# Kernel optimization log

Hardware: AMD Instinct MI355X
Metric: run time of the kernel (lower is better)

The kernel has to match this reference:

```python
import jax, jax.numpy as jnp
import numpy as np

N_PATCHES = 262144
N_BAGS = 32
INPUT_DIM = 1024
FEAT_DIM = 256
ATTN_DIM = 128
HEAD_DIM = 2


def setup_inputs() -> dict:
    key = jax.random.key(0)
    ks = jax.random.split(key, 9)
    s = 0.02
    return {
        "features": jax.random.normal(ks[0], (N_PATCHES, INPUT_DIM), jnp.float32),
        "W1": jax.random.normal(ks[1], (FEAT_DIM, INPUT_DIM), jnp.float32) * s,
        "b1": jnp.zeros((FEAT_DIM,), jnp.float32),
        "Wa1": jax.random.normal(ks[2], (ATTN_DIM, FEAT_DIM), jnp.float32) * s,
        "ba1": jnp.zeros((ATTN_DIM,), jnp.float32),
        "Wa2": jax.random.normal(ks[3], (1, ATTN_DIM), jnp.float32) * s,
        "ba2": jnp.zeros((1,), jnp.float32),
        "Wh": jax.random.normal(ks[4], (HEAD_DIM, FEAT_DIM), jnp.float32) * s,
        "bh": jnp.zeros((HEAD_DIM,), jnp.float32),
        "bag_sizes": jnp.full((N_BAGS,), N_PATCHES // N_BAGS, jnp.int32),
    }


def reference(features, W1, b1, Wa1, ba1, Wa2, ba2, Wh, bh, bag_sizes):
    # encoder: Linear(input_dim -> features_dim) + ReLU
    h = jax.nn.relu(features @ W1.T + b1)                        # [N, F]
    # attention MLP: Linear -> tanh -> Linear -> scalar score
    a = jnp.tanh(h @ Wa1.T + ba1)                                # [N, A]
    scores = (a @ Wa2.T + ba2)[:, 0]                             # [N]
    # segmented softmax over bags + attention-weighted reduce
    seg = jnp.repeat(jnp.arange(N_BAGS), bag_sizes, total_repeat_length=N_PATCHES)
    m = jax.ops.segment_max(scores, seg, num_segments=N_BAGS)    # [B]
    e = jnp.exp(scores - m[seg])                                 # [N]
    z = jax.ops.segment_sum(e, seg, num_segments=N_BAGS)         # [B]
    attn = e / z[seg]                                            # [N]
    bag_emb = jax.ops.segment_sum(attn[:, None] * h, seg, num_segments=N_BAGS)  # [B, F]
    # linear head
    return bag_emb @ Wh.T + bh                                   # [B, head_dim]
```

## Files before the change

kernel.cpp:

```cpp
#include <hip/hip_runtime.h>
#include <cstdint>
#include <cstddef>

typedef short short8 __attribute__((ext_vector_type(8)));
typedef float f32x4 __attribute__((ext_vector_type(4)));
typedef int   i32x4 __attribute__((ext_vector_type(4)));

#define NPATCH 262144
#define NBAGS  32
#define IN_DIM 1024
#define F_DIM  256
#define A_DIM  128
#define ROWSB  128
#define NBLK   (NPATCH / ROWSB)

__device__ __forceinline__ unsigned short f2bf(float f){
  uint32_t u = __builtin_bit_cast(uint32_t, f);
  u += 0x7fffu + ((u >> 16) & 1u);
  return (unsigned short)(u >> 16);
}
__device__ __forceinline__ float bf2f(unsigned short h){
  return __builtin_bit_cast(float, (uint32_t)h << 16);
}
__device__ __forceinline__ float tanh_fast(float x){
  float e = __expf(2.f * x);
  return (e - 1.f) * __builtin_amdgcn_rcpf(e + 1.f);
}
__device__ __forceinline__ uint32_t cvtpk(float a, float b){
  uint32_t r;
  asm("v_cvt_pk_bf16_f32 %0, %1, %2" : "=v"(r) : "v"(a), "v"(b));
  return r;
}
__device__ __forceinline__ void gload_lds16(const void* g, void* l){
  __builtin_amdgcn_global_load_lds((const __attribute__((address_space(1))) void*)g,
                                   (__attribute__((address_space(3))) void*)l, 16, 0, 0);
}

#define MFMA(a,b,c) __builtin_amdgcn_mfma_f32_16x16x32_bf16((a),(b),(c),0,0,0)
#define SWZ4(r)  (((r) & 3) << 4)
#define SWZH(r)  (((r) & 7) << 4)

__global__ void prep_kernel(const float* __restrict__ W1, const float* __restrict__ Wa1,
                            unsigned short* __restrict__ w1b, unsigned short* __restrict__ wa1b,
                            float* __restrict__ bagAcc){
  int id = blockIdx.x * 256 + threadIdx.x;
  if (id < F_DIM*IN_DIM) {
    w1b[id] = f2bf(W1[id]);
  } else if (id < F_DIM*IN_DIM + A_DIM*F_DIM) {
    int j = id - F_DIM*IN_DIM;
    wa1b[j] = f2bf(Wa1[j]);
  } else if (id < F_DIM*IN_DIM + A_DIM*F_DIM + NBAGS*257) {
    bagAcc[id - (F_DIM*IN_DIM + A_DIM*F_DIM)] = 0.f;
  }
}

__global__ __launch_bounds__(256, 2)
void mil_main(const float* __restrict__ feat,
              const unsigned short* __restrict__ w1b,
              const float* __restrict__ b1,
              const unsigned short* __restrict__ wa1b,
              const float* __restrict__ ba1,
              const float* __restrict__ wa2,
              const float* __restrict__ ba2v,
              float* __restrict__ bagAcc)
{
  extern __shared__ char lds[];
  char* Abuf[2] = { lds, lds + 8192 };
  char* Bbuf[2] = { lds + 16384, lds + 32768 };
  char* HsB  = lds;
  float* sc4  = (float*)(lds + 65536);
  float* evec = (float*)(lds + 65536 + 2048);
  float* Pp   = (float*)(lds + 65536 + 2048 + 512);

  const int tid  = threadIdx.x;
  const int wid  = tid >> 6;
  const int lane = tid & 63;
  const int l15  = lane & 15;
  const int l4   = lane >> 4;
  const int wm   = wid >> 1;
  const int wn   = wid & 1;
  const int bRow = blockIdx.x * ROWSB;

  const int arow = tid >> 1;
  const int ahalf = tid & 1;
  const float* aG = feat + (size_t)(bRow + arow) * IN_DIM + ahalf * 16;
  const int awb = arow * 64 + ahalf * 32;
  const int aswz = SWZ4(arow);

  const char* srcB[4];
  #pragma unroll
  for (int i = 0; i < 4; ++i){
    int Blin = wid*4096 + i*1024 + lane*16;
    int col  = Blin >> 6;
    int kb   = Blin & 63;
    srcB[i] = (const char*)w1b + (size_t)col*2048 + (kb ^ SWZ4(col));
  }

#define STAGEB(bb, t) do { \
    _Pragma("unroll") \
    for (int i_ = 0; i_ < 4; ++i_) \
      gload_lds16(srcB[i_] + (size_t)(t)*64, (bb) + wid*4096 + i_*1024); \
  } while(0)

#define LOADT(R, t) do { \
    const float* p_ = aG + (t)*32; \
    R[0] = *(const float4*)(p_ + 0);  R[1] = *(const float4*)(p_ + 4); \
    R[2] = *(const float4*)(p_ + 8);  R[3] = *(const float4*)(p_ + 12); \
  } while(0)

#define CVTST(R, ab) do { \
    const float* v_ = (const float*)(R); \
    i32x4 w0_ = { (int)cvtpk(v_[0],  v_[1]),  (int)cvtpk(v_[2],  v_[3]), \
                  (int)cvtpk(v_[4],  v_[5]),  (int)cvtpk(v_[6],  v_[7]) }; \
    i32x4 w1_ = { (int)cvtpk(v_[8],  v_[9]),  (int)cvtpk(v_[10], v_[11]), \
                  (int)cvtpk(v_[12], v_[13]), (int)cvtpk(v_[14], v_[15]) }; \
    *(i32x4*)((ab) + ((awb +  0) ^ aswz)) = w0_; \
    *(i32x4*)((ab) + ((awb + 16) ^ aswz)) = w1_; \
  } while(0)

#define COMPUTE(ab, bb) do { \
    short8 af_[4], bf_[8]; \
    _Pragma("unroll") \
    for (int mf_ = 0; mf_ < 4; ++mf_){ \
      int row_ = wm*64 + mf_*16 + l15; \
      af_[mf_] = *(const short8*)((ab) + (row_*64 + ((l4*16) ^ SWZ4(row_)))); \
    } \
    _Pragma("unroll") \
    for (int nf_ = 0; nf_ < 8; ++nf_){ \
      int col_ = wn*128 + nf_*16 + l15; \
      bf_[nf_] = *(const short8*)((bb) + (col_*64 + ((l4*16) ^ SWZ4(col_)))); \
    } \
    _Pragma("unroll") \
    for (int mf_ = 0; mf_ < 4; ++mf_) \
      _Pragma("unroll") \
      for (int nf_ = 0; nf_ < 8; ++nf_) \
        acc[mf_][nf_] = MFMA(af_[mf_], bf_[nf_], acc[mf_][nf_]); \
  } while(0)

#define KBAR(N) do { \
    asm volatile("s_waitcnt vmcnt(" #N ") lgkmcnt(0)" ::: "memory"); \
    __builtin_amdgcn_sched_barrier(0); \
    __builtin_amdgcn_s_barrier(); \
  } while(0)

  f32x4 acc[4][8];
  #pragma unroll
  for (int i = 0; i < 4; ++i)
    #pragma unroll
    for (int j = 0; j < 8; ++j) acc[i][j] = (f32x4){0.f, 0.f, 0.f, 0.f};

  float4 aR0[4], aR1[4];

  STAGEB(Bbuf[0], 0);
  LOADT(aR0, 0);
  LOADT(aR1, 1);
  CVTST(aR0, Abuf[0]);
  KBAR(0);

  for (int tp = 0; tp < 15; ++tp){
    const int t0 = tp*2, t1 = tp*2 + 1;
    STAGEB(Bbuf[1], t0 + 1);
    LOADT(aR0, t0 + 2);
    __builtin_amdgcn_sched_barrier(0);
    COMPUTE(Abuf[0], Bbuf[0]);
    CVTST(aR1, Abuf[1]);
    KBAR(4);
    STAGEB(Bbuf[0], t1 + 1);
    if (t1 + 2 < 32) LOADT(aR1, t1 + 2);
    __builtin_amdgcn_sched_barrier(0);
    COMPUTE(Abuf[1], Bbuf[1]);
    CVTST(aR0, Abuf[0]);
    KBAR(4);
  }
  STAGEB(Bbuf[1], 31);
  COMPUTE(Abuf[0], Bbuf[0]);
  CVTST(aR1, Abuf[1]);
  KBAR(0);
  COMPUTE(Abuf[1], Bbuf[1]);
  __syncthreads();

  float b1v[8];
  #pragma unroll
  for (int nf = 0; nf < 8; ++nf) b1v[nf] = b1[wn*128 + nf*16 + l15];

  #pragma unroll
  for (int mf = 0; mf < 4; ++mf)
    #pragma unroll
    for (int nf = 0; nf < 8; ++nf)
      #pragma unroll
      for (int r = 0; r < 4; ++r){
        int row = wm*64 + mf*16 + l4*4 + r;
        int col = wn*128 + nf*16 + l15;
        float v = fmaxf(acc[mf][nf][r] + b1v[nf], 0.f);
        int by = (row*512 + col*2) ^ SWZH(row);
        *(unsigned short*)(HsB + by) = f2bf(v);
      }
  __syncthreads();

  f32x4 acc2[8][2];
  #pragma unroll
  for (int i = 0; i < 8; ++i)
    #pragma unroll
    for (int j = 0; j < 2; ++j) acc2[i][j] = (f32x4){0.f, 0.f, 0.f, 0.f};

  #pragma unroll
  for (int ks2 = 0; ks2 < 8; ++ks2){
    short8 hf[8], wf[2];
    #pragma unroll
    for (int mf = 0; mf < 8; ++mf){
      int row = mf*16 + l15;
      int by  = (row*512 + (ks2*32 + l4*8)*2) ^ SWZH(row);
      hf[mf] = *(const short8*)(HsB + by);
    }
    #pragma unroll
    for (int nf = 0; nf < 2; ++nf){
      int col = wid*32 + nf*16 + l15;
      wf[nf] = *(const short8*)(const void*)(wa1b + col*256 + ks2*32 + l4*8);
    }
    #pragma unroll
    for (int mf = 0; mf < 8; ++mf)
      #pragma unroll
      for (int nf = 0; nf < 2; ++nf)
        acc2[mf][nf] = MFMA(hf[mf], wf[nf], acc2[mf][nf]);
  }

  float ba1v[2], wa2v[2];
  #pragma unroll
  for (int nf = 0; nf < 2; ++nf){
    int col = wid*32 + nf*16 + l15;
    ba1v[nf] = ba1[col];
    wa2v[nf] = wa2[col];
  }
  #pragma unroll
  for (int mf = 0; mf < 8; ++mf)
    #pragma unroll
    for (int r = 0; r < 4; ++r){
      float p = tanh_fast(acc2[mf][0][r] + ba1v[0]) * wa2v[0]
              + tanh_fast(acc2[mf][1][r] + ba1v[1]) * wa2v[1];
      p += __shfl_xor(p, 1);
      p += __shfl_xor(p, 2);
      p += __shfl_xor(p, 4);
      p += __shfl_xor(p, 8);
      if (l15 == 0){
        int row = mf*16 + l4*4 + r;
        sc4[row*4 + wid] = p;
      }
    }
  __syncthreads();

  if (tid < 128){
    float s = sc4[tid*4+0] + sc4[tid*4+1] + sc4[tid*4+2] + sc4[tid*4+3] + ba2v[0];
    evec[tid] = __expf(s);
  }
  __syncthreads();

  {
    const int f0 = (tid & 127) << 1;
    const int g  = tid >> 7;
    float p0 = 0.f, p1 = 0.f;
    const int rbase = g << 6;
    #pragma unroll 8
    for (int i = 0; i < 64; ++i){
      const int r = rbase + i;
      const uint32_t hw = *(const uint32_t*)(HsB + ((r*512 + f0*2) ^ SWZH(r)));
      const float e = evec[r];
      p0 = fmaf(e, bf2f((unsigned short)(hw & 0xffffu)), p0);
      p1 = fmaf(e, bf2f((unsigned short)(hw >> 16)),     p1);
    }
    Pp[(g << 8) + f0]     = p0;
    Pp[(g << 8) + f0 + 1] = p1;
  }
  __syncthreads();

  const int bag = bRow >> 13;
  {
    float s = Pp[tid] + Pp[256 + tid];
    atomicAdd(&bagAcc[bag*257 + tid], s);
  }
  if (tid < 64){
    float se = evec[tid] + evec[tid + 64];
    se += __shfl_xor(se, 1);
    se += __shfl_xor(se, 2);
    se += __shfl_xor(se, 4);
    se += __shfl_xor(se, 8);
    se += __shfl_xor(se, 16);
    se += __shfl_xor(se, 32);
    if (tid == 0) atomicAdd(&bagAcc[bag*257 + 256], se);
  }
#undef STAGEB
#undef LOADT
#undef CVTST
#undef COMPUTE
#undef KBAR
}

__global__ void head_kernel(const float* __restrict__ bagAcc,
                            const float* __restrict__ wh,
                            const float* __restrict__ bh,
                            float* __restrict__ out){
  int t = threadIdx.x;
  int b = t >> 1, d = t & 1;
  const float* P = bagAcc + b*257;
  float invE = 1.f / P[256];
  float acc = 0.f;
  for (int f = 0; f < 256; ++f) acc += P[f] * wh[d*256 + f];
  out[b*2 + d] = acc * invE + bh[d];
}

extern "C" void kernel_launch(void* const* d_in, const int* in_sizes, int n_in,
                              void* d_out, int out_size, void* d_ws, size_t ws_size,
                              hipStream_t stream){
  const float* feat = (const float*)d_in[0];
  const float* W1   = (const float*)d_in[1];
  const float* b1   = (const float*)d_in[2];
  const float* Wa1  = (const float*)d_in[3];
  const float* ba1  = (const float*)d_in[4];
  const float* Wa2  = (const float*)d_in[5];
  const float* ba2  = (const float*)d_in[6];
  const float* Wh   = (const float*)d_in[7];
  const float* bh   = (const float*)d_in[8];

  unsigned short* w1b  = (unsigned short*)d_ws;
  unsigned short* wa1b = (unsigned short*)((char*)d_ws + 524288);
  float* bagAcc        = (float*)((char*)d_ws + 589824);

  prep_kernel<<<1185, 256, 0, stream>>>(W1, Wa1, w1b, wa1b, bagAcc);

  const size_t ldsBytes = 65536 + 2048 + 512 + 2048;
  mil_main<<<NBLK, 256, ldsBytes, stream>>>(feat, w1b, b1, wa1b, ba1,
                                            Wa2, ba2, bagAcc);

  head_kernel<<<1, 64, 0, stream>>>(bagAcc, Wh, bh, (float*)d_out);
}
```

Baseline: 337.4 us.

## Split fused MIL kernel into GEMM1 and attention kernels with direct fp32 LDS loads

Splits the fused kernel into a GEMM1+ReLU kernel that writes bf16 hidden activations to a workspace buffer and a separate attention/pooling kernel that reads them back into LDS. GEMM1 now loads fp32 features straight into LDS asynchronously and converts them to bf16 when building fragments, instead of staging through registers. GEMM1 also uses less LDS so it can run at higher occupancy. The cost is an extra global round trip of the hidden activations, plus a single-buffered A tile that waits for all outstanding loads every step.

```diff
diff --git a/kernel.cpp b/kernel.cpp
--- a/kernel.cpp
+++ b/kernel.cpp
@@ -37,8 +37,9 @@
 }
 
 #define MFMA(a,b,c) __builtin_amdgcn_mfma_f32_16x16x32_bf16((a),(b),(c),0,0,0)
-#define SWZ4(r)  (((r) & 3) << 4)
-#define SWZH(r)  (((r) & 7) << 4)
+#define SWZA(r) (((r) & 7) << 4)
+#define SWZB(c) (((c) & 3) << 4)
+#define SWZH(r) (((r) & 7) << 4)
 
 __global__ void prep_kernel(const float* __restrict__ W1, const float* __restrict__ Wa1,
                             unsigned short* __restrict__ w1b, unsigned short* __restrict__ wa1b,
@@ -54,23 +55,16 @@
   }
 }
 
-__global__ __launch_bounds__(256, 2)
-void mil_main(const float* __restrict__ feat,
-              const unsigned short* __restrict__ w1b,
-              const float* __restrict__ b1,
-              const unsigned short* __restrict__ wa1b,
-              const float* __restrict__ ba1,
-              const float* __restrict__ wa2,
-              const float* __restrict__ ba2v,
-              float* __restrict__ bagAcc)
+__global__ __launch_bounds__(256, 3)
+void gemm1_kernel(const float* __restrict__ feat,
+                  const unsigned short* __restrict__ w1b,
+                  const float* __restrict__ b1,
+                  unsigned short* __restrict__ hout)
 {
   extern __shared__ char lds[];
-  char* Abuf[2] = { lds, lds + 8192 };
-  char* Bbuf[2] = { lds + 16384, lds + 32768 };
-  char* HsB  = lds;
-  float* sc4  = (float*)(lds + 65536);
-  float* evec = (float*)(lds + 65536 + 2048);
-  float* Pp   = (float*)(lds + 65536 + 2048 + 512);
+  char* Abuf  = lds;
+  char* Bbuf0 = lds + 16384;
+  char* Bbuf1 = lds + 32768;
 
   const int tid  = threadIdx.x;
   const int wid  = tid >> 6;
@@ -81,103 +75,77 @@
   const int wn   = wid & 1;
   const int bRow = blockIdx.x * ROWSB;
 
-  const int arow = tid >> 1;
-  const int ahalf = tid & 1;
-  const float* aG = feat + (size_t)(bRow + arow) * IN_DIM + ahalf * 16;
-  const int awb = arow * 64 + ahalf * 32;
-  const int aswz = SWZ4(arow);
-
+  const char* srcA[4];
   const char* srcB[4];
   #pragma unroll
   for (int i = 0; i < 4; ++i){
     int Blin = wid*4096 + i*1024 + lane*16;
-    int col  = Blin >> 6;
-    int kb   = Blin & 63;
-    srcB[i] = (const char*)w1b + (size_t)col*2048 + (kb ^ SWZ4(col));
-  }
-
-#define STAGEB(bb, t) do { \
+    int arow = Blin >> 7;
+    int acb  = (Blin & 127) ^ SWZA(arow);
+    srcA[i] = (const char*)feat + (size_t)(bRow + arow)*4096 + acb;
+    int bcol = Blin >> 6;
+    int bkb  = (Blin & 63) ^ SWZB(bcol);
+    srcB[i] = (const char*)w1b + (size_t)bcol*2048 + bkb;
+  }
+
+#define GLOADA(t) do { \
+    _Pragma("unroll") \
+    for (int i_ = 0; i_ < 4; ++i_) \
+      gload_lds16(srcA[i_] + (size_t)(t)*128, Abuf + wid*4096 + i_*1024); \
+  } while(0)
+#define GLOADB(bb, t) do { \
     _Pragma("unroll") \
     for (int i_ = 0; i_ < 4; ++i_) \
       gload_lds16(srcB[i_] + (size_t)(t)*64, (bb) + wid*4096 + i_*1024); \
   } while(0)
 
-#define LOADT(R, t) do { \
-    const float* p_ = aG + (t)*32; \
-    R[0] = *(const float4*)(p_ + 0);  R[1] = *(const float4*)(p_ + 4); \
-    R[2] = *(const float4*)(p_ + 8);  R[3] = *(const float4*)(p_ + 12); \
-  } while(0)
-
-#define CVTST(R, ab) do { \
-    const float* v_ = (const float*)(R); \
-    i32x4 w0_ = { (int)cvtpk(v_[0],  v_[1]),  (int)cvtpk(v_[2],  v_[3]), \
-                  (int)cvtpk(v_[4],  v_[5]),  (int)cvtpk(v_[6],  v_[7]) }; \
-    i32x4 w1_ = { (int)cvtpk(v_[8],  v_[9]),  (int)cvtpk(v_[10], v_[11]), \
-                  (int)cvtpk(v_[12], v_[13]), (int)cvtpk(v_[14], v_[15]) }; \
-    *(i32x4*)((ab) + ((awb +  0) ^ aswz)) = w0_; \
-    *(i32x4*)((ab) + ((awb + 16) ^ aswz)) = w1_; \
-  } while(0)
-
-#define COMPUTE(ab, bb) do { \
-    short8 af_[4], bf_[8]; \
+  f32x4 acc[4][8];
+  #pragma unroll
+  for (int i = 0; i < 4; ++i)
+    #pragma unroll
+    for (int j = 0; j < 8; ++j) acc[i][j] = (f32x4){0.f, 0.f, 0.f, 0.f};
+
+  GLOADA(0);
+  GLOADB(Bbuf0, 0);
+
+#define STEP(T, CUR, NXT, DONEXT) do { \
+     \
+    asm volatile("s_waitcnt vmcnt(0)" ::: "memory"); \
+    __builtin_amdgcn_sched_barrier(0); \
+    __builtin_amdgcn_s_barrier(); \
+    short8 af_[4]; \
     _Pragma("unroll") \
     for (int mf_ = 0; mf_ < 4; ++mf_){ \
       int row_ = wm*64 + mf_*16 + l15; \
-      af_[mf_] = *(const short8*)((ab) + (row_*64 + ((l4*16) ^ SWZ4(row_)))); \
+      int p0_  = row_*128 + ((l4*32) ^ SWZA(row_)); \
+      f32x4 lo_ = *(const f32x4*)(Abuf + p0_); \
+      f32x4 hi_ = *(const f32x4*)(Abuf + (p0_ ^ 16)); \
+      i32x4 t4_ = { (int)cvtpk(lo_[0], lo_[1]), (int)cvtpk(lo_[2], lo_[3]), \
+                    (int)cvtpk(hi_[0], hi_[1]), (int)cvtpk(hi_[2], hi_[3]) }; \
+      af_[mf_] = __builtin_bit_cast(short8, t4_); \
     } \
+    asm volatile("s_waitcnt lgkmcnt(0)" ::: "memory"); \
+    __builtin_amdgcn_sched_barrier(0); \
+    __builtin_amdgcn_s_barrier();                     \
+    if (DONEXT){ GLOADA((T) + 1); GLOADB(NXT, (T) + 1); } \
+    __builtin_amdgcn_sched_barrier(0); \
     _Pragma("unroll") \
     for (int nf_ = 0; nf_ < 8; ++nf_){ \
       int col_ = wn*128 + nf_*16 + l15; \
-      bf_[nf_] = *(const short8*)((bb) + (col_*64 + ((l4*16) ^ SWZ4(col_)))); \
+      short8 bf_ = *(const short8*)((CUR) + (col_*64 + ((l4*16) ^ SWZB(col_)))); \
+      _Pragma("unroll") \
+      for (int mf_ = 0; mf_ < 4; ++mf_) \
+        acc[mf_][nf_] = MFMA(af_[mf_], bf_, acc[mf_][nf_]); \
     } \
-    _Pragma("unroll") \
-    for (int mf_ = 0; mf_ < 4; ++mf_) \
-      _Pragma("unroll") \
-      for (int nf_ = 0; nf_ < 8; ++nf_) \
-        acc[mf_][nf_] = MFMA(af_[mf_], bf_[nf_], acc[mf_][nf_]); \
   } while(0)
 
-#define KBAR(N) do { \
-    asm volatile("s_waitcnt vmcnt(" #N ") lgkmcnt(0)" ::: "memory"); \
-    __builtin_amdgcn_sched_barrier(0); \
-    __builtin_amdgcn_s_barrier(); \
-  } while(0)
-
-  f32x4 acc[4][8];
-  #pragma unroll
-  for (int i = 0; i < 4; ++i)
-    #pragma unroll
-    for (int j = 0; j < 8; ++j) acc[i][j] = (f32x4){0.f, 0.f, 0.f, 0.f};
-
-  float4 aR0[4], aR1[4];
-
-  STAGEB(Bbuf[0], 0);
-  LOADT(aR0, 0);
-  LOADT(aR1, 1);
-  CVTST(aR0, Abuf[0]);
-  KBAR(0);
-
-  for (int tp = 0; tp < 15; ++tp){
-    const int t0 = tp*2, t1 = tp*2 + 1;
-    STAGEB(Bbuf[1], t0 + 1);
-    LOADT(aR0, t0 + 2);
-    __builtin_amdgcn_sched_barrier(0);
-    COMPUTE(Abuf[0], Bbuf[0]);
-    CVTST(aR1, Abuf[1]);
-    KBAR(4);
-    STAGEB(Bbuf[0], t1 + 1);
-    if (t1 + 2 < 32) LOADT(aR1, t1 + 2);
-    __builtin_amdgcn_sched_barrier(0);
-    COMPUTE(Abuf[1], Bbuf[1]);
-    CVTST(aR0, Abuf[0]);
-    KBAR(4);
-  }
-  STAGEB(Bbuf[1], 31);
-  COMPUTE(Abuf[0], Bbuf[0]);
-  CVTST(aR1, Abuf[1]);
-  KBAR(0);
-  COMPUTE(Abuf[1], Bbuf[1]);
-  __syncthreads();
+  for (int tt = 0; tt < 16; ++tt){
+    STEP(2*tt,     Bbuf0, Bbuf1, 1);
+    STEP(2*tt + 1, Bbuf1, Bbuf0, (tt < 15));
+  }
+#undef STEP
+#undef GLOADA
+#undef GLOADB
 
   float b1v[8];
   #pragma unroll
@@ -192,9 +160,41 @@
         int row = wm*64 + mf*16 + l4*4 + r;
         int col = wn*128 + nf*16 + l15;
         float v = fmaxf(acc[mf][nf][r] + b1v[nf], 0.f);
-        int by = (row*512 + col*2) ^ SWZH(row);
-        *(unsigned short*)(HsB + by) = f2bf(v);
+        hout[(size_t)(bRow + row)*256 + col] = f2bf(v);
       }
+}
+
+__global__ __launch_bounds__(256, 2)
+void attn_kernel(const unsigned short* __restrict__ hin,
+                 const unsigned short* __restrict__ wa1b,
+                 const float* __restrict__ ba1,
+                 const float* __restrict__ wa2,
+                 const float* __restrict__ ba2v,
+                 float* __restrict__ bagAcc)
+{
+  extern __shared__ char lds[];
+  char* HsB  = lds;
+  float* sc4  = (float*)(lds + 65536);
+  float* evec = (float*)(lds + 65536 + 2048);
+  float* Pp   = (float*)(lds + 65536 + 2048 + 512);
+
+  const int tid  = threadIdx.x;
+  const int wid  = tid >> 6;
+  const int lane = tid & 63;
+  const int l15  = lane & 15;
+  const int l4   = lane >> 4;
+  const int bRow = blockIdx.x * ROWSB;
+
+  #pragma unroll
+  for (int i = 0; i < 16; ++i){
+    int Blin = wid*16384 + i*1024 + lane*16;
+    int row  = Blin >> 9;
+    int colb = (Blin & 511) ^ SWZH(row);
+    gload_lds16((const char*)hin + (size_t)(bRow + row)*512 + colb,
+                HsB + wid*16384 + i*1024);
+  }
+  asm volatile("s_waitcnt vmcnt(0)" ::: "memory");
+  __builtin_amdgcn_sched_barrier(0);
   __syncthreads();
 
   f32x4 acc2[8][2];
@@ -287,11 +287,6 @@
     se += __shfl_xor(se, 32);
     if (tid == 0) atomicAdd(&bagAcc[bag*257 + 256], se);
   }
-#undef STAGEB
-#undef LOADT
-#undef CVTST
-#undef COMPUTE
-#undef KBAR
 }
 
 __global__ void head_kernel(const float* __restrict__ bagAcc,
@@ -323,12 +318,13 @@
   unsigned short* w1b  = (unsigned short*)d_ws;
   unsigned short* wa1b = (unsigned short*)((char*)d_ws + 524288);
   float* bagAcc        = (float*)((char*)d_ws + 589824);
+  unsigned short* hbuf = (unsigned short*)((char*)d_ws + 1048576);
 
   prep_kernel<<<1185, 256, 0, stream>>>(W1, Wa1, w1b, wa1b, bagAcc);
 
-  const size_t ldsBytes = 65536 + 2048 + 512 + 2048;
-  mil_main<<<NBLK, 256, ldsBytes, stream>>>(feat, w1b, b1, wa1b, ba1,
-                                            Wa2, ba2, bagAcc);
+  gemm1_kernel<<<NBLK, 256, 49152, stream>>>(feat, w1b, b1, hbuf);
+
+  attn_kernel<<<NBLK, 256, 70144, stream>>>(hbuf, wa1b, ba1, Wa2, ba2, bagAcc);
 
   head_kernel<<<1, 64, 0, stream>>>(bagAcc, Wh, bh, (float*)d_out);
 }
```

Measured after the change: 642.3 us. 1.9x slower.

## Halve rows per block to 64 and raise occupancy to three blocks per CU

Applied to the files above, without the earlier changes.

Cuts the per-block row tile from 128 to 64, which halves the A staging buffers, accumulators and H scratch, so LDS per block falls to about 40KB and the launch bound allows three blocks per CU. The MFMA loop now interleaves B-fragment loads with the MFMAs to lower register pressure, and the pipeline waits on fewer outstanding loads per step. The cost is twice as many blocks, each streaming the whole W1 weight matrix, so weight traffic from L2 doubles and there are twice as many atomics, while each loaded B fragment now feeds two MFMAs instead of four. Memory-bound loading of the fp32 features may gain from the extra wavefronts in flight.

```diff
diff --git a/kernel.cpp b/kernel.cpp
--- a/kernel.cpp
+++ b/kernel.cpp
@@ -11,7 +11,7 @@
 #define IN_DIM 1024
 #define F_DIM  256
 #define A_DIM  128
-#define ROWSB  128
+#define ROWSB  64
 #define NBLK   (NPATCH / ROWSB)
 
 __device__ __forceinline__ unsigned short f2bf(float f){
@@ -37,8 +37,8 @@
 }
 
 #define MFMA(a,b,c) __builtin_amdgcn_mfma_f32_16x16x32_bf16((a),(b),(c),0,0,0)
-#define SWZ4(r)  (((r) & 3) << 4)
-#define SWZH(r)  (((r) & 7) << 4)
+#define SWZ4(r) (((r) & 3) << 4)
+#define SWZH(r) (((r) & 7) << 4)
 
 __global__ void prep_kernel(const float* __restrict__ W1, const float* __restrict__ Wa1,
                             unsigned short* __restrict__ w1b, unsigned short* __restrict__ wa1b,
@@ -54,7 +54,7 @@
   }
 }
 
-__global__ __launch_bounds__(256, 2)
+__global__ __launch_bounds__(256, 3)
 void mil_main(const float* __restrict__ feat,
               const unsigned short* __restrict__ w1b,
               const float* __restrict__ b1,
@@ -65,12 +65,14 @@
               float* __restrict__ bagAcc)
 {
   extern __shared__ char lds[];
-  char* Abuf[2] = { lds, lds + 8192 };
-  char* Bbuf[2] = { lds + 16384, lds + 32768 };
-  char* HsB  = lds;
-  float* sc4  = (float*)(lds + 65536);
-  float* evec = (float*)(lds + 65536 + 2048);
-  float* Pp   = (float*)(lds + 65536 + 2048 + 512);
+  char* Abuf0 = lds;
+  char* Abuf1 = lds + 4096;
+  char* Bbuf0 = lds + 8192;
+  char* Bbuf1 = lds + 24576;
+  char* HsB   = lds;
+  float* sc4  = (float*)(lds + 32768);
+  float* evec = (float*)(lds + 32768 + 1024);
+  float* Pp   = (float*)(lds + 32768 + 1024 + 256);
 
   const int tid  = threadIdx.x;
   const int wid  = tid >> 6;
@@ -81,19 +83,18 @@
   const int wn   = wid & 1;
   const int bRow = blockIdx.x * ROWSB;
 
-  const int arow = tid >> 1;
-  const int ahalf = tid & 1;
-  const float* aG = feat + (size_t)(bRow + arow) * IN_DIM + ahalf * 16;
-  const int awb = arow * 64 + ahalf * 32;
-  const int aswz = SWZ4(arow);
+  const int ar = tid >> 2;
+  const int as = tid & 3;
+  const float* aG = feat + (size_t)(bRow + ar) * IN_DIM + as * 8;
+  const int awb = (ar * 64 + as * 16) ^ SWZ4(ar);
 
   const char* srcB[4];
   #pragma unroll
   for (int i = 0; i < 4; ++i){
     int Blin = wid*4096 + i*1024 + lane*16;
     int col  = Blin >> 6;
-    int kb   = Blin & 63;
-    srcB[i] = (const char*)w1b + (size_t)col*2048 + (kb ^ SWZ4(col));
+    int kb   = (Blin & 63) ^ SWZ4(col);
+    srcB[i] = (const char*)w1b + (size_t)col*2048 + kb;
   }
 
 #define STAGEB(bb, t) do { \
@@ -104,37 +105,30 @@
 
 #define LOADT(R, t) do { \
     const float* p_ = aG + (t)*32; \
-    R[0] = *(const float4*)(p_ + 0);  R[1] = *(const float4*)(p_ + 4); \
-    R[2] = *(const float4*)(p_ + 8);  R[3] = *(const float4*)(p_ + 12); \
+    R[0] = *(const float4*)p_;  R[1] = *(const float4*)(p_ + 4); \
   } while(0)
 
 #define CVTST(R, ab) do { \
     const float* v_ = (const float*)(R); \
-    i32x4 w0_ = { (int)cvtpk(v_[0],  v_[1]),  (int)cvtpk(v_[2],  v_[3]), \
-                  (int)cvtpk(v_[4],  v_[5]),  (int)cvtpk(v_[6],  v_[7]) }; \
-    i32x4 w1_ = { (int)cvtpk(v_[8],  v_[9]),  (int)cvtpk(v_[10], v_[11]), \
-                  (int)cvtpk(v_[12], v_[13]), (int)cvtpk(v_[14], v_[15]) }; \
-    *(i32x4*)((ab) + ((awb +  0) ^ aswz)) = w0_; \
-    *(i32x4*)((ab) + ((awb + 16) ^ aswz)) = w1_; \
+    i32x4 w_ = { (int)cvtpk(v_[0], v_[1]), (int)cvtpk(v_[2], v_[3]), \
+                 (int)cvtpk(v_[4], v_[5]), (int)cvtpk(v_[6], v_[7]) }; \
+    *(i32x4*)((ab) + awb) = w_; \
   } while(0)
 
 #define COMPUTE(ab, bb) do { \
-    short8 af_[4], bf_[8]; \
+    short8 af_[2]; \
     _Pragma("unroll") \
-    for (int mf_ = 0; mf_ < 4; ++mf_){ \
-      int row_ = wm*64 + mf_*16 + l15; \
+    for (int mf_ = 0; mf_ < 2; ++mf_){ \
+      int row_ = wm*32 + mf_*16 + l15; \
       af_[mf_] = *(const short8*)((ab) + (row_*64 + ((l4*16) ^ SWZ4(row_)))); \
     } \
     _Pragma("unroll") \
     for (int nf_ = 0; nf_ < 8; ++nf_){ \
       int col_ = wn*128 + nf_*16 + l15; \
-      bf_[nf_] = *(const short8*)((bb) + (col_*64 + ((l4*16) ^ SWZ4(col_)))); \
+      short8 bf_ = *(const short8*)((bb) + (col_*64 + ((l4*16) ^ SWZ4(col_)))); \
+      acc[0][nf_] = MFMA(af_[0], bf_, acc[0][nf_]); \
+      acc[1][nf_] = MFMA(af_[1], bf_, acc[1][nf_]); \
     } \
-    _Pragma("unroll") \
-    for (int mf_ = 0; mf_ < 4; ++mf_) \
-      _Pragma("unroll") \
-      for (int nf_ = 0; nf_ < 8; ++nf_) \
-        acc[mf_][nf_] = MFMA(af_[mf_], bf_[nf_], acc[mf_][nf_]); \
   } while(0)
 
 #define KBAR(N) do { \
@@ -143,53 +137,60 @@
     __builtin_amdgcn_s_barrier(); \
   } while(0)
 
-  f32x4 acc[4][8];
-  #pragma unroll
-  for (int i = 0; i < 4; ++i)
+  f32x4 acc[2][8];
+  #pragma unroll
+  for (int i = 0; i < 2; ++i)
     #pragma unroll
     for (int j = 0; j < 8; ++j) acc[i][j] = (f32x4){0.f, 0.f, 0.f, 0.f};
 
-  float4 aR0[4], aR1[4];
-
-  STAGEB(Bbuf[0], 0);
+  float4 aR0[2], aR1[2];
+
+  STAGEB(Bbuf0, 0);
   LOADT(aR0, 0);
   LOADT(aR1, 1);
-  CVTST(aR0, Abuf[0]);
+  CVTST(aR0, Abuf0);
+  KBAR(2);
+
+#define STEP(T, AC, BC, AN, BN, ARC, ARN, W) do { \
+    STAGEB(BN, (T) + 1); \
+    __builtin_amdgcn_sched_barrier(0); \
+    if ((T) + 2 < 32) LOADT(ARC, (T) + 2); \
+    __builtin_amdgcn_sched_barrier(0); \
+    COMPUTE(AC, BC); \
+    CVTST(ARN, AN); \
+    KBAR(W); \
+  } while(0)
+
+  for (int tp = 0; tp < 15; ++tp){
+    const int t0 = tp*2;
+    STEP(t0,     Abuf0, Bbuf0, Abuf1, Bbuf1, aR0, aR1, 2);
+    STEP(t0 + 1, Abuf1, Bbuf1, Abuf0, Bbuf0, aR1, aR0, 2);
+  }
+  STAGEB(Bbuf1, 31);
+  COMPUTE(Abuf0, Bbuf0);
+  CVTST(aR1, Abuf1);
   KBAR(0);
-
-  for (int tp = 0; tp < 15; ++tp){
-    const int t0 = tp*2, t1 = tp*2 + 1;
-    STAGEB(Bbuf[1], t0 + 1);
-    LOADT(aR0, t0 + 2);
-    __builtin_amdgcn_sched_barrier(0);
-    COMPUTE(Abuf[0], Bbuf[0]);
-    CVTST(aR1, Abuf[1]);
-    KBAR(4);
-    STAGEB(Bbuf[0], t1 + 1);
-    if (t1 + 2 < 32) LOADT(aR1, t1 + 2);
-    __builtin_amdgcn_sched_barrier(0);
-    COMPUTE(Abuf[1], Bbuf[1]);
-    CVTST(aR0, Abuf[0]);
-    KBAR(4);
-  }
-  STAGEB(Bbuf[1], 31);
-  COMPUTE(Abuf[0], Bbuf[0]);
-  CVTST(aR1, Abuf[1]);
-  KBAR(0);
-  COMPUTE(Abuf[1], Bbuf[1]);
-  __syncthreads();
+  COMPUTE(Abuf1, Bbuf1);
+  __syncthreads();
+
+#undef STEP
+#undef STAGEB
+#undef LOADT
+#undef CVTST
+#undef COMPUTE
+#undef KBAR
 
   float b1v[8];
   #pragma unroll
   for (int nf = 0; nf < 8; ++nf) b1v[nf] = b1[wn*128 + nf*16 + l15];
 
   #pragma unroll
-  for (int mf = 0; mf < 4; ++mf)
+  for (int mf = 0; mf < 2; ++mf)
     #pragma unroll
     for (int nf = 0; nf < 8; ++nf)
       #pragma unroll
       for (int r = 0; r < 4; ++r){
-        int row = wm*64 + mf*16 + l4*4 + r;
+        int row = wm*32 + mf*16 + l4*4 + r;
         int col = wn*128 + nf*16 + l15;
         float v = fmaxf(acc[mf][nf][r] + b1v[nf], 0.f);
         int by = (row*512 + col*2) ^ SWZH(row);
@@ -197,17 +198,17 @@
       }
   __syncthreads();
 
-  f32x4 acc2[8][2];
-  #pragma unroll
-  for (int i = 0; i < 8; ++i)
+  f32x4 acc2[4][2];
+  #pragma unroll
+  for (int i = 0; i < 4; ++i)
     #pragma unroll
     for (int j = 0; j < 2; ++j) acc2[i][j] = (f32x4){0.f, 0.f, 0.f, 0.f};
 
   #pragma unroll
   for (int ks2 = 0; ks2 < 8; ++ks2){
-    short8 hf[8], wf[2];
-    #pragma unroll
-    for (int mf = 0; mf < 8; ++mf){
+    short8 hf[4], wf[2];
+    #pragma unroll
+    for (int mf = 0; mf < 4; ++mf){
       int row = mf*16 + l15;
       int by  = (row*512 + (ks2*32 + l4*8)*2) ^ SWZH(row);
       hf[mf] = *(const short8*)(HsB + by);
@@ -218,7 +219,7 @@
       wf[nf] = *(const short8*)(const void*)(wa1b + col*256 + ks2*32 + l4*8);
     }
     #pragma unroll
-    for (int mf = 0; mf < 8; ++mf)
+    for (int mf = 0; mf < 4; ++mf)
       #pragma unroll
       for (int nf = 0; nf < 2; ++nf)
         acc2[mf][nf] = MFMA(hf[mf], wf[nf], acc2[mf][nf]);
@@ -232,7 +233,7 @@
     wa2v[nf] = wa2[col];
   }
   #pragma unroll
-  for (int mf = 0; mf < 8; ++mf)
+  for (int mf = 0; mf < 4; ++mf)
     #pragma unroll
     for (int r = 0; r < 4; ++r){
       float p = tanh_fast(acc2[mf][0][r] + ba1v[0]) * wa2v[0]
@@ -248,7 +249,7 @@
     }
   __syncthreads();
 
-  if (tid < 128){
+  if (tid < 64){
     float s = sc4[tid*4+0] + sc4[tid*4+1] + sc4[tid*4+2] + sc4[tid*4+3] + ba2v[0];
     evec[tid] = __expf(s);
   }
@@ -258,9 +259,9 @@
     const int f0 = (tid & 127) << 1;
     const int g  = tid >> 7;
     float p0 = 0.f, p1 = 0.f;
-    const int rbase = g << 6;
+    const int rbase = g << 5;
     #pragma unroll 8
-    for (int i = 0; i < 64; ++i){
+    for (int i = 0; i < 32; ++i){
       const int r = rbase + i;
       const uint32_t hw = *(const uint32_t*)(HsB + ((r*512 + f0*2) ^ SWZH(r)));
       const float e = evec[r];
@@ -278,7 +279,7 @@
     atomicAdd(&bagAcc[bag*257 + tid], s);
   }
   if (tid < 64){
-    float se = evec[tid] + evec[tid + 64];
+    float se = evec[tid];
     se += __shfl_xor(se, 1);
     se += __shfl_xor(se, 2);
     se += __shfl_xor(se, 4);
@@ -287,11 +288,6 @@
     se += __shfl_xor(se, 32);
     if (tid == 0) atomicAdd(&bagAcc[bag*257 + 256], se);
   }
-#undef STAGEB
-#undef LOADT
-#undef CVTST
-#undef COMPUTE
-#undef KBAR
 }
 
 __global__ void head_kernel(const float* __restrict__ bagAcc,
@@ -326,9 +322,8 @@
 
   prep_kernel<<<1185, 256, 0, stream>>>(W1, Wa1, w1b, wa1b, bagAcc);
 
-  const size_t ldsBytes = 65536 + 2048 + 512 + 2048;
-  mil_main<<<NBLK, 256, ldsBytes, stream>>>(feat, w1b, b1, wa1b, ba1,
-                                            Wa2, ba2, bagAcc);
+  mil_main<<<NBLK, 256, 40960, stream>>>(feat, w1b, b1, wa1b, ba1,
+                                         Wa2, ba2, bagAcc);
 
   head_kernel<<<1, 64, 0, stream>>>(bagAcc, Wh, bh, (float*)d_out);
 }
```

After: 377.4 us. 1.12x slower.
